# Optimization experiments

Hardware: AMD Instinct MI355X
Metric: run time of the kernel (lower is better)

Reference implementation:

```python
import jax, jax.numpy as jnp
import numpy as np

B, T, I, H = 4096, 2048, 3, 32


def setup_inputs() -> dict:
    key = jax.random.key(0)
    k1, k2, k3, k4, k5 = jax.random.split(key, 5)
    s = 1.0 / np.sqrt(H)  # PyTorch LSTM init scale
    return {
        "x": jax.random.normal(k1, (B, T, I), dtype=jnp.float32),
        "W_ih": jax.random.uniform(k2, (4 * H, I), jnp.float32, -s, s),
        "W_hh": jax.random.uniform(k3, (4 * H, H), jnp.float32, -s, s),
        "b_ih": jax.random.uniform(k4, (4 * H,), jnp.float32, -s, s),
        "b_hh": jax.random.uniform(k5, (4 * H,), jnp.float32, -s, s),
    }


def reference(x, W_ih, W_hh, b_ih, b_hh):
    # Precompute input contribution to all gates: [T, B, 4H]
    xg = jnp.einsum("bti,gi->tbg", x, W_ih) + (b_ih + b_hh)
    h0 = jnp.zeros((x.shape[0], H), dtype=x.dtype)
    c0 = jnp.zeros((x.shape[0], H), dtype=x.dtype)

    def step(carry, xg_t):
        h, c = carry
        gates = xg_t + h @ W_hh.T  # [B, 4H]
        i, f, g, o = jnp.split(gates, 4, axis=-1)  # PyTorch gate order i,f,g,o
        i = jax.nn.sigmoid(i)
        f = jax.nn.sigmoid(f)
        g = jnp.tanh(g)
        o = jax.nn.sigmoid(o)
        c_new = f * c + i * g
        h_new = o * jnp.tanh(c_new)
        return (h_new, c_new), None

    (h_final, _), _ = jax.lax.scan(step, (h0, c0), xg)
    return h_final  # equivalent to h[-1] in the torch module: [B, H]
```

## Files before the change

### kernel.cpp

```cpp
#include <hip/hip_runtime.h>

namespace {
constexpr int T = 2048;
constexpr int B = 4096;
constexpr int H = 32;
constexpr int GPB = 8;

__device__ __forceinline__ float fsigmoid(float x) {
  return __builtin_amdgcn_rcpf(1.0f + __expf(-x));
}
__device__ __forceinline__ float ftanh_(float x) {
  return 2.0f * __builtin_amdgcn_rcpf(1.0f + __expf(-2.0f * x)) - 1.0f;
}
}

__global__ __launch_bounds__(256, 2)
void lstm_fused(const float* __restrict__ x,
                const float* __restrict__ W_ih,
                const float* __restrict__ W_hh,
                const float* __restrict__ b_ih,
                const float* __restrict__ b_hh,
                float* __restrict__ out)
{
  const int j   = threadIdx.x & 31;
  const int grp = threadIdx.x >> 5;
  const int b   = blockIdx.x * GPB + grp;

  float wi[H], wf[H], wg[H], wo[H];
  {
    const float4* Wv = reinterpret_cast<const float4*>(W_hh);
    #pragma unroll
    for (int q = 0; q < H / 4; ++q) {
      float4 a = Wv[(0 * H + j) * (H / 4) + q];
      wi[4*q+0] = a.x; wi[4*q+1] = a.y; wi[4*q+2] = a.z; wi[4*q+3] = a.w;
      float4 f4 = Wv[(1 * H + j) * (H / 4) + q];
      wf[4*q+0] = f4.x; wf[4*q+1] = f4.y; wf[4*q+2] = f4.z; wf[4*q+3] = f4.w;
      float4 g4 = Wv[(2 * H + j) * (H / 4) + q];
      wg[4*q+0] = g4.x; wg[4*q+1] = g4.y; wg[4*q+2] = g4.z; wg[4*q+3] = g4.w;
      float4 o4 = Wv[(3 * H + j) * (H / 4) + q];
      wo[4*q+0] = o4.x; wo[4*q+1] = o4.y; wo[4*q+2] = o4.z; wo[4*q+3] = o4.w;
    }
  }
  const float ui0 = W_ih[(0*H+j)*3+0], ui1 = W_ih[(0*H+j)*3+1], ui2 = W_ih[(0*H+j)*3+2];
  const float uf0 = W_ih[(1*H+j)*3+0], uf1 = W_ih[(1*H+j)*3+1], uf2 = W_ih[(1*H+j)*3+2];
  const float ug0 = W_ih[(2*H+j)*3+0], ug1 = W_ih[(2*H+j)*3+1], ug2 = W_ih[(2*H+j)*3+2];
  const float uo0 = W_ih[(3*H+j)*3+0], uo1 = W_ih[(3*H+j)*3+1], uo2 = W_ih[(3*H+j)*3+2];
  const float bi  = b_ih[0*H+j] + b_hh[0*H+j];
  const float bf_ = b_ih[1*H+j] + b_hh[1*H+j];
  const float bg  = b_ih[2*H+j] + b_hh[2*H+j];
  const float bo  = b_ih[3*H+j] + b_hh[3*H+j];

  float h = 0.0f, c = 0.0f;
  const float* xb = x + (size_t)b * T * 3;

  for (int tc = 0; tc < T; tc += 32) {
    const float* xp = xb + (size_t)(tc + j) * 3;
    float xl0 = xp[0], xl1 = xp[1], xl2 = xp[2];
    #pragma unroll 4
    for (int s = 0; s < 32; ++s) {
      float x0 = __shfl(xl0, s, 32);
      float x1 = __shfl(xl1, s, 32);
      float x2 = __shfl(xl2, s, 32);
      float pi = __builtin_fmaf(x0, ui0, __builtin_fmaf(x1, ui1, __builtin_fmaf(x2, ui2, bi )));
      float pf = __builtin_fmaf(x0, uf0, __builtin_fmaf(x1, uf1, __builtin_fmaf(x2, uf2, bf_)));
      float pg = __builtin_fmaf(x0, ug0, __builtin_fmaf(x1, ug1, __builtin_fmaf(x2, ug2, bg )));
      float po = __builtin_fmaf(x0, uo0, __builtin_fmaf(x1, uo1, __builtin_fmaf(x2, uo2, bo )));
      #pragma unroll
      for (int k = 0; k < H; ++k) {
        float hk = __shfl(h, k, 32);
        pi = __builtin_fmaf(hk, wi[k], pi);
        pf = __builtin_fmaf(hk, wf[k], pf);
        pg = __builtin_fmaf(hk, wg[k], pg);
        po = __builtin_fmaf(hk, wo[k], po);
      }
      float ig = fsigmoid(pi);
      float fg = fsigmoid(pf);
      float gg = ftanh_(pg);
      float og = fsigmoid(po);
      c = __builtin_fmaf(fg, c, ig * gg);
      h = og * ftanh_(c);
    }
  }
  out[b * H + j] = h;
}

extern "C" void kernel_launch(void* const* d_in, const int* in_sizes, int n_in,
                              void* d_out, int out_size, void* d_ws, size_t ws_size,
                              hipStream_t stream) {
  const float* x    = (const float*)d_in[0];
  const float* W_ih = (const float*)d_in[1];
  const float* W_hh = (const float*)d_in[2];
  const float* b_ih = (const float*)d_in[3];
  const float* b_hh = (const float*)d_in[4];
  float* out = (float*)d_out;

  dim3 grid(B / GPB), block(256);
  hipLaunchKernelGGL(lstm_fused, grid, block, 0, stream,
                     x, W_ih, W_hh, b_ih, b_hh, out);
}
```

Measured before the change: 1.776 ms.

## Split LSTM gates across full 64-lane wave with packed FMA and LDS h broadcast

Each batch row now uses a full 64-lane wave instead of 32 lanes. The low half computes the i and g gates and the high half computes f and o, using packed two-wide FMAs. The hidden state is broadcast through LDS as duplicated pairs read with float4 loads, replacing 32 per-step shuffles. Weights are pre-scaled by -log2(e) so the activations use exp2 directly. This halves per-lane FMA work and registers, allowing higher occupancy, at the cost of relying on wave-synchronous LDS ordering with only compiler fences and no barriers.

```diff
diff --git a/kernel.cpp b/kernel.cpp
--- a/kernel.cpp
+++ b/kernel.cpp
@@ -1,20 +1,23 @@
 #include <hip/hip_runtime.h>
+
+typedef float v2 __attribute__((ext_vector_type(2)));
+
+#define MEMFENCE() asm volatile("" ::: "memory")
 
 namespace {
 constexpr int T = 2048;
 constexpr int B = 4096;
 constexpr int H = 32;
-constexpr int GPB = 8;
+constexpr int WAVES = 4;
+constexpr int CHUNK = 64;
 
-__device__ __forceinline__ float fsigmoid(float x) {
-  return __builtin_amdgcn_rcpf(1.0f + __expf(-x));
-}
-__device__ __forceinline__ float ftanh_(float x) {
-  return 2.0f * __builtin_amdgcn_rcpf(1.0f + __expf(-2.0f * x)) - 1.0f;
-}
+struct WaveLds {
+  v2 hdup[H];
+  float4 xbuf[CHUNK];
+};
 }
 
-__global__ __launch_bounds__(256, 2)
+__global__ __launch_bounds__(256, 4)
 void lstm_fused(const float* __restrict__ x,
                 const float* __restrict__ W_ih,
                 const float* __restrict__ W_hh,
@@ -22,66 +25,94 @@
                 const float* __restrict__ b_hh,
                 float* __restrict__ out)
 {
-  const int j   = threadIdx.x & 31;
-  const int grp = threadIdx.x >> 5;
-  const int b   = blockIdx.x * GPB + grp;
+  __shared__ WaveLds lds[WAVES];
+  const int lane = threadIdx.x & 63;
+  const int wid  = threadIdx.x >> 6;
+  const int j    = lane & 31;
+  const bool low = lane < 32;
+  const int b    = blockIdx.x * WAVES + wid;
+  WaveLds& L = lds[wid];
 
-  float wi[H], wf[H], wg[H], wo[H];
+  const int g0 = (low ? 0 : 1) * H + j;
+  const int g1 = (low ? 2 : 3) * H + j;
+
+  const float L2E = 1.442695040888963f;
+  const float s0 = -L2E;
+  const float s1 = low ? -2.0f * L2E : -L2E;
+  const float k2 = low ? 2.0f : 1.0f;
+  const float k3 = low ? -1.0f : 0.0f;
+
+  v2 wpk[H];
   {
-    const float4* Wv = reinterpret_cast<const float4*>(W_hh);
+    const float4* r0 = reinterpret_cast<const float4*>(W_hh + g0 * H);
+    const float4* r1 = reinterpret_cast<const float4*>(W_hh + g1 * H);
     #pragma unroll
     for (int q = 0; q < H / 4; ++q) {
-      float4 a = Wv[(0 * H + j) * (H / 4) + q];
-      wi[4*q+0] = a.x; wi[4*q+1] = a.y; wi[4*q+2] = a.z; wi[4*q+3] = a.w;
-      float4 f4 = Wv[(1 * H + j) * (H / 4) + q];
-      wf[4*q+0] = f4.x; wf[4*q+1] = f4.y; wf[4*q+2] = f4.z; wf[4*q+3] = f4.w;
-      float4 g4 = Wv[(2 * H + j) * (H / 4) + q];
-      wg[4*q+0] = g4.x; wg[4*q+1] = g4.y; wg[4*q+2] = g4.z; wg[4*q+3] = g4.w;
-      float4 o4 = Wv[(3 * H + j) * (H / 4) + q];
-      wo[4*q+0] = o4.x; wo[4*q+1] = o4.y; wo[4*q+2] = o4.z; wo[4*q+3] = o4.w;
+      float4 a = r0[q], d = r1[q];
+      wpk[4*q+0] = v2{a.x * s0, d.x * s1};
+      wpk[4*q+1] = v2{a.y * s0, d.y * s1};
+      wpk[4*q+2] = v2{a.z * s0, d.z * s1};
+      wpk[4*q+3] = v2{a.w * s0, d.w * s1};
     }
   }
-  const float ui0 = W_ih[(0*H+j)*3+0], ui1 = W_ih[(0*H+j)*3+1], ui2 = W_ih[(0*H+j)*3+2];
-  const float uf0 = W_ih[(1*H+j)*3+0], uf1 = W_ih[(1*H+j)*3+1], uf2 = W_ih[(1*H+j)*3+2];
-  const float ug0 = W_ih[(2*H+j)*3+0], ug1 = W_ih[(2*H+j)*3+1], ug2 = W_ih[(2*H+j)*3+2];
-  const float uo0 = W_ih[(3*H+j)*3+0], uo1 = W_ih[(3*H+j)*3+1], uo2 = W_ih[(3*H+j)*3+2];
-  const float bi  = b_ih[0*H+j] + b_hh[0*H+j];
-  const float bf_ = b_ih[1*H+j] + b_hh[1*H+j];
-  const float bg  = b_ih[2*H+j] + b_hh[2*H+j];
-  const float bo  = b_ih[3*H+j] + b_hh[3*H+j];
+  const v2 u0 = {W_ih[g0*3+0] * s0, W_ih[g1*3+0] * s1};
+  const v2 u1 = {W_ih[g0*3+1] * s0, W_ih[g1*3+1] * s1};
+  const v2 u2 = {W_ih[g0*3+2] * s0, W_ih[g1*3+2] * s1};
+  const v2 bias = {(b_ih[g0] + b_hh[g0]) * s0, (b_ih[g1] + b_hh[g1]) * s1};
 
-  float h = 0.0f, c = 0.0f;
+  L.hdup[j] = v2{0.f, 0.f};
+  MEMFENCE();
+
+  float c = 0.f, h = 0.f;
   const float* xb = x + (size_t)b * T * 3;
+  const float4* hd4 = reinterpret_cast<const float4*>(L.hdup);
 
-  for (int tc = 0; tc < T; tc += 32) {
-    const float* xp = xb + (size_t)(tc + j) * 3;
-    float xl0 = xp[0], xl1 = xp[1], xl2 = xp[2];
-    #pragma unroll 4
-    for (int s = 0; s < 32; ++s) {
-      float x0 = __shfl(xl0, s, 32);
-      float x1 = __shfl(xl1, s, 32);
-      float x2 = __shfl(xl2, s, 32);
-      float pi = __builtin_fmaf(x0, ui0, __builtin_fmaf(x1, ui1, __builtin_fmaf(x2, ui2, bi )));
-      float pf = __builtin_fmaf(x0, uf0, __builtin_fmaf(x1, uf1, __builtin_fmaf(x2, uf2, bf_)));
-      float pg = __builtin_fmaf(x0, ug0, __builtin_fmaf(x1, ug1, __builtin_fmaf(x2, ug2, bg )));
-      float po = __builtin_fmaf(x0, uo0, __builtin_fmaf(x1, uo1, __builtin_fmaf(x2, uo2, bo )));
+  for (int tcb = 0; tcb < T; tcb += CHUNK) {
+    MEMFENCE();
+    const float* xp = xb + (size_t)(tcb + lane) * 3;
+    L.xbuf[lane] = make_float4(xp[0], xp[1], xp[2], 0.f);
+    MEMFENCE();
+
+    #pragma unroll 2
+    for (int s = 0; s < CHUNK; ++s) {
+      const float4 xv = L.xbuf[s];
+      v2 accA = bias;
+      v2 accB = {0.f, 0.f};
+      accA = __builtin_elementwise_fma(v2{xv.x, xv.x}, u0, accA);
+      accB = __builtin_elementwise_fma(v2{xv.y, xv.y}, u1, accB);
+      accA = __builtin_elementwise_fma(v2{xv.z, xv.z}, u2, accA);
       #pragma unroll
-      for (int k = 0; k < H; ++k) {
-        float hk = __shfl(h, k, 32);
-        pi = __builtin_fmaf(hk, wi[k], pi);
-        pf = __builtin_fmaf(hk, wf[k], pf);
-        pg = __builtin_fmaf(hk, wg[k], pg);
-        po = __builtin_fmaf(hk, wo[k], po);
+      for (int q = 0; q < H / 2; ++q) {
+        float4 hh = hd4[q];
+        accA = __builtin_elementwise_fma(v2{hh.x, hh.y}, wpk[2*q+0], accA);
+        accB = __builtin_elementwise_fma(v2{hh.z, hh.w}, wpk[2*q+1], accB);
       }
-      float ig = fsigmoid(pi);
-      float fg = fsigmoid(pf);
-      float gg = ftanh_(pg);
-      float og = fsigmoid(po);
-      c = __builtin_fmaf(fg, c, ig * gg);
-      h = og * ftanh_(c);
+      v2 acc = accA + accB;
+
+      float e0 = __builtin_amdgcn_exp2f(acc.x);
+      float v0 = __builtin_amdgcn_rcpf(1.f + e0);
+      float e1 = __builtin_amdgcn_exp2f(acc.y);
+      float v1 = __builtin_fmaf(__builtin_amdgcn_rcpf(1.f + e1), k2, k3);
+
+      float p0 = __shfl_xor(v0, 32, 64);
+      float p1 = __shfl_xor(v1, 32, 64);
+      float sf = low ? p0 : v0;
+      float si = low ? v0 : p0;
+      float so = low ? p1 : v1;
+      float tg = low ? v1 : p1;
+
+      c = __builtin_fmaf(sf, c, si * tg);
+      float ec = __builtin_amdgcn_exp2f(c * (-2.0f * L2E));
+      float th = __builtin_fmaf(__builtin_amdgcn_rcpf(1.f + ec), 2.f, -1.f);
+      h = so * th;
+
+      MEMFENCE();
+      L.hdup[j] = v2{h, h};
+      MEMFENCE();
     }
   }
-  out[b * H + j] = h;
+
+  if (low) out[(size_t)b * H + j] = h;
 }
 
 extern "C" void kernel_launch(void* const* d_in, const int* in_sizes, int n_in,
@@ -94,7 +125,7 @@
   const float* b_hh = (const float*)d_in[4];
   float* out = (float*)d_out;
 
-  dim3 grid(B / GPB), block(256);
+  dim3 grid(B / WAVES), block(256);
   hipLaunchKernelGGL(lstm_fused, grid, block, 0, stream,
                      x, W_ih, W_hh, b_ih, b_hh, out);
 }
```

Result: faster. 1.589 ms (-10.5%).
